# Kernel optimization log

Measured on AMD Instinct MI355X. Metric: run time of the kernel, lower is better.

Reference implementation:

```python
import jax, jax.numpy as jnp
import numpy as np

H = 256
N = 64           # d_state; diagonal SSM uses N//2 conjugate-pair modes
N2 = N // 2
B, L = 16, 4096
EPS = 1e-5


def layernorm(x, g, b):
    m = jnp.mean(x, axis=-1, keepdims=True)
    v = jnp.mean((x - m) ** 2, axis=-1, keepdims=True)
    return (x - m) / jnp.sqrt(v + EPS) * g + b


def s4_layer(u, log_dt, A_re, A_im, C_re, C_im, D, Wout, bout):
    # u: (B, L, H). Bidirectional diagonal S4 (S4D-style ZOH kernel), channels=1.
    Bb, Ll, Hh = u.shape
    dt = jnp.exp(log_dt)                       # (H,)
    A = A_re + 1j * A_im                       # (H, N2), Re(A) < 0
    dtA = dt[:, None] * A                      # (H, N2)
    # ZOH discretization folded into C:  C <- C * (exp(dtA) - 1) / A
    C = (C_re + 1j * C_im) * (jnp.exp(dtA) - 1.0) / A   # (2, H, N2)
    vand = jnp.exp(dtA[:, :, None] * jnp.arange(Ll))    # (H, N2, L)
    k = 2.0 * jnp.einsum('chn,hnl->chl', C, vand).real  # (2, H, L)
    k_fwd, k_bwd = k[0], k[1]
    # bidirectional: causal kernel + anticausal (flipped, shifted by L)
    z = jnp.zeros_like(k_fwd)
    k2 = jnp.concatenate([k_fwd, z], axis=-1) \
       + jnp.concatenate([z, k_bwd[:, ::-1]], axis=-1)  # (H, 2L)
    ut = jnp.transpose(u, (0, 2, 1))                    # (B, H, L)
    n_fft = 2 * Ll
    y = jnp.fft.irfft(jnp.fft.rfft(ut, n=n_fft) * jnp.fft.rfft(k2, n=n_fft), n=n_fft)[..., :Ll]
    y = y + ut * D[:, None]                             # skip connection
    y = jax.nn.gelu(y, approximate=False)
    y = jnp.transpose(y, (0, 2, 1))                     # (B, L, H)
    zz = y @ Wout + bout                                # (B, L, 2H)
    return zz[..., :Hh] * jax.nn.sigmoid(zz[..., Hh:])  # GLU output projection


def setup_inputs() -> dict:
    key = jax.random.key(0)
    ks = jax.random.split(key, 16)
    x = jax.random.normal(ks[0], (B, L, H), dtype=jnp.float32)
    log_dt = jnp.log(0.001) + jax.random.uniform(ks[1], (H,)) * (jnp.log(0.1) - jnp.log(0.001))
    A_re = -0.5 * jnp.ones((H, N2), dtype=jnp.float32)
    A_im = jnp.pi * jnp.broadcast_to(jnp.arange(N2, dtype=jnp.float32), (H, N2))
    C_re = jax.random.normal(ks[2], (2, H, N2), dtype=jnp.float32) * 0.5
    C_im = jax.random.normal(ks[3], (2, H, N2), dtype=jnp.float32) * 0.5
    Dskip = jax.random.normal(ks[4], (H,), dtype=jnp.float32)
    Wout = jax.random.normal(ks[5], (H, 2 * H), dtype=jnp.float32) / np.sqrt(H)
    bout = jnp.zeros((2 * H,), dtype=jnp.float32)
    ln1_g = jnp.ones((H,), jnp.float32); ln1_b = jnp.zeros((H,), jnp.float32)
    ln2_g = jnp.ones((H,), jnp.float32); ln2_b = jnp.zeros((H,), jnp.float32)
    W2 = jax.random.normal(ks[6], (H, 2 * H), dtype=jnp.float32) / np.sqrt(H)
    b2 = jnp.zeros((2 * H,), jnp.float32)
    W3 = jax.random.normal(ks[7], (2 * H, H), dtype=jnp.float32) / np.sqrt(2 * H)
    b3 = jnp.zeros((H,), jnp.float32)
    return dict(x=x, ln1_g=ln1_g, ln1_b=ln1_b, ln2_g=ln2_g, ln2_b=ln2_b,
                log_dt=log_dt, A_re=A_re, A_im=A_im, C_re=C_re, C_im=C_im,
                Dskip=Dskip, Wout=Wout, bout=bout, W2=W2, b2=b2, W3=W3, b3=b3)


def reference(x, ln1_g, ln1_b, ln2_g, ln2_b, log_dt, A_re, A_im, C_re, C_im,
              Dskip, Wout, bout, W2, b2, W3, b3):
    # residual S4 sub-block
    y = x
    h = layernorm(x, ln1_g, ln1_b)
    h = s4_layer(h, log_dt, A_re, A_im, C_re, C_im, Dskip, Wout, bout)
    x = y + h
    # residual MLP sub-block
    y = x
    h = layernorm(x, ln2_g, ln2_b)
    h = jax.nn.gelu(h @ W2 + b2, approximate=False)
    h = h @ W3 + b3
    return y + h
```

## Files before the change

### kernel.cpp

```cpp
#include <hip/hip_runtime.h>
#include <hip/hip_bf16.h>

typedef __attribute__((ext_vector_type(8))) short bf16x8;
typedef __attribute__((ext_vector_type(4))) float f32x4;

#define Hdim 256
#define NM 32
#define NB 16
#define LL 4096
#define PCH 256
#define NCH 16

#define OFF_Q    ((size_t)0)
#define OFF_KC   ((size_t)16777216)
#define OFF_WPM  ((size_t)50331648)
#define OFF_UT   ((size_t)67108864)
#define OFF_ZG   ((size_t)100663296)
#define OFF_M    ((size_t)67108864)
#define OFF_ZP   ((size_t)134217728)
#define OFF_G    ((size_t)150994944)
#define OFF_WTAB ((size_t)185073664)
#define OFF_WPT  ((size_t)185139200)
#define OFF_CE   ((size_t)185204736)
#define OFF_W1T  ((size_t)185335808)
#define OFF_W2T  ((size_t)185597952)
#define OFF_W3T  ((size_t)185860096)

typedef const __attribute__((address_space(1))) void* gas_p;
typedef __attribute__((address_space(3))) void* las_p;

__device__ __forceinline__ float gelu_f(float v) {
    float u = 0.7978845608028654f * fmaf(0.044715f * v * v, v, v);
    float uc = fminf(fmaxf(u, -15.f), 15.f);
    float e = __expf(2.f * uc);
    return 0.5f * v * (1.f + (e - 1.f) * __builtin_amdgcn_rcpf(e + 1.f));
}
__device__ __forceinline__ unsigned short f2bf(float f) {
    unsigned int u = __float_as_uint(f);
    u += 0x7fffu + ((u >> 16) & 1u);
    return (unsigned short)(u >> 16);
}
__device__ __forceinline__ float bf2f(unsigned short u) {
    return __uint_as_float((unsigned int)u << 16);
}

__device__ __forceinline__ bf16x8 fr(const unsigned short* lds, int row, int kcol) {
    return *(const bf16x8*)(lds + row * 64 + ((((kcol >> 3) ^ (row & 7)) << 3)));
}

template<int ROWS, int THREADS>
__device__ __forceinline__ void stage64(const unsigned short* __restrict__ src, int ld, int k0,
                                        unsigned short* lds, int t) {
    constexpr int EPI = THREADS * 8;
#pragma unroll
    for (int i = 0; i < (ROWS * 64) / EPI; i++) {
        int e = i * EPI + t * 8;
        int r = e >> 6;
        int k = (((e >> 3) & 7) ^ (r & 7)) << 3;
        const unsigned short* g = src + (size_t)r * ld + (k0 + k);
        unsigned short* l = lds + i * EPI + (t >> 6) * 512;
        __builtin_amdgcn_global_load_lds((gas_p)g, (las_p)l, 16, 0, 0);
    }
}

template<int ROWS, int THREADS>
__device__ __forceinline__ void stageUT(const unsigned short* __restrict__ UT, int h, int rbase,
                                        int k0, unsigned short* lds, int t) {
    constexpr int EPI = THREADS * 8;
#pragma unroll
    for (int i = 0; i < (ROWS * 64) / EPI; i++) {
        int e = i * EPI + t * 8;
        int r = e >> 6;
        int k = (((e >> 3) & 7) ^ (r & 7)) << 3;
        int row = rbase + r;
        const unsigned short* g = UT + ((size_t)((row >> 4) * Hdim + h)) * LL
                                  + (row & 15) * PCH + (k0 + k);
        unsigned short* l = lds + i * EPI + (t >> 6) * 512;
        __builtin_amdgcn_global_load_lds((gas_p)g, (las_p)l, 16, 0, 0);
    }
}

__global__ void k_tab(const float* __restrict__ logdt, const float* __restrict__ Are,
                      const float* __restrict__ Aim, const float* __restrict__ Cre,
                      const float* __restrict__ Cim, float2* __restrict__ wtab,
                      float2* __restrict__ wptab, float2* __restrict__ ceff) {
    int idx = blockIdx.x * blockDim.x + threadIdx.x;
    if (idx >= Hdim * NM) return;
    int h = idx >> 5;
    float dt = expf(logdt[h]);
    double dar = (double)dt * (double)Are[idx];
    double dai = (double)dt * (double)Aim[idx];
    double wm = exp(dar);
    double wr = wm * cos(dai), wi = wm * sin(dai);
    wtab[idx] = make_float2((float)wr, (float)wi);
    double pm = exp(dar * (double)PCH);
    double pai = dai * (double)PCH;
    wptab[idx] = make_float2((float)(pm * cos(pai)), (float)(pm * sin(pai)));
    double are = (double)Are[idx], aim = (double)Aim[idx];
    double den = are * are + aim * aim;
    double nr = wr - 1.0, ni = wi;
    double qr = (nr * are + ni * aim) / den;
    double qi = (ni * are - nr * aim) / den;
    for (int ch = 0; ch < 2; ch++) {
        double cr = (double)Cre[ch * Hdim * NM + idx];
        double ci = (double)Cim[ch * Hdim * NM + idx];
        ceff[ch * Hdim * NM + idx] = make_float2((float)(cr * qr - ci * qi),
                                                 (float)(cr * qi + ci * qr));
    }
}

__global__ void k_wt(const float* __restrict__ W1, const float* __restrict__ W2,
                     const float* __restrict__ W3, unsigned short* __restrict__ W1T,
                     unsigned short* __restrict__ W2T, unsigned short* __restrict__ W3T) {
    int t = blockIdx.x * 256 + threadIdx.x;
    int k = t >> 9, n = t & 511;
    W1T[n * 256 + k] = f2bf(W1[t]);
    W2T[n * 256 + k] = f2bf(W2[t]);
    int k3 = t >> 8, n3 = t & 255;
    W3T[n3 * 512 + k3] = f2bf(W3[t]);
}

__global__ __launch_bounds__(256) void k_abw(const float* __restrict__ logdt,
                                             const float* __restrict__ Are,
                                             const float* __restrict__ Aim,
                                             const float2* __restrict__ CE,
                                             unsigned short* __restrict__ Q,
                                             unsigned short* __restrict__ Wp,
                                             float* __restrict__ Kcat) {
    __shared__ float2 wpow[32][258];
    __shared__ float2 ce_s[64];
    int h = blockIdx.x;
    int part = blockIdx.y;
    int t = threadIdx.x;
    if (t < 64) ce_s[t] = CE[(t >> 5) * (Hdim * NM) + h * NM + (t & 31)];
    {
        int n = t >> 3, seg = t & 7;
        float dt = expf(logdt[h]);
        float dar = dt * Are[h * NM + n], dai = dt * Aim[h * NM + n];
        float em = expf(dar);
        float wr = em * cosf(dai), wi = em * sinf(dai);
        float ar = wr, ai = wi;
#pragma unroll
        for (int s = 0; s < 3; s++) { float nr = ar * ar - ai * ai, ni = 2.f * ar * ai; ar = nr; ai = ni; }
        float m = expf((float)seg * dar), ang = (float)seg * dai;
        float vr = m * cosf(ang), vi = m * sinf(ang);
        for (int q = 0; q < 32; q++) {
            wpow[n][seg + 8 * q] = make_float2(vr, vi);
            float nr2 = vr * ar - vi * ai;
            float ni2 = vr * ai + vi * ar;
            vr = nr2; vi = ni2;
        }
        if (seg == 0) wpow[n][256] = make_float2(vr, vi);
    }
    __syncthreads();
    if (part == 4) {
        float kfv = 0.f, kbv = 0.f;
#pragma unroll
        for (int n = 0; n < NM; n++) {
            float2 wv = wpow[n][t];
            float2 cf = ce_s[n], cb = ce_s[32 + n];
            kfv = fmaf(cf.x, wv.x, fmaf(-cf.y, wv.y, kfv));
            kbv = fmaf(cb.x, wv.x, fmaf(-cb.y, wv.y, kbv));
        }
        Kcat[(size_t)h * 512 + 255 + t] = 2.f * kfv;
        if (t < 255) Kcat[(size_t)h * 512 + 254 - t] = 2.f * kbv;
        if (t == 255) Kcat[(size_t)h * 512 + 511] = 0.f;
        return;
    }
    for (int jj = 0; jj < 32; jj++) {
        int j = part * 64 + jj * 2 + (t >> 7);
        int tq = t & 127;
        int n = (tq & 63) >> 1, reim = tq & 1;
        float2 c = (tq < 64) ? ce_s[n] : ce_s[32 + n];
        float2 wv = (tq < 64) ? wpow[n][j + 1] : wpow[n][255 - j];
        float re = c.x * wv.x - c.y * wv.y;
        float im = c.x * wv.y + c.y * wv.x;
        Q[((size_t)h * 256 + j) * 128 + tq] = f2bf(reim ? -2.f * im : 2.f * re);
    }
    for (int rr = 0; rr < 32; rr++) {
        int r = part * 32 + rr;
        int n = (r & 63) >> 1, reim = r & 1, dir = r >> 6;
        float2 wv = wpow[n][dir ? t : 255 - t];
        Wp[((size_t)h * 128 + r) * 256 + t] = f2bf(reim ? wv.y : wv.x);
    }
}

__global__ __launch_bounds__(256) void k_lntr(const float* __restrict__ x,
                                              const float* __restrict__ g,
                                              const float* __restrict__ bt,
                                              unsigned short* __restrict__ UT) {
    __shared__ unsigned short lds[256][65];
    int lt = blockIdx.x, b = blockIdx.y;
    int t = threadIdx.x;
    int lane = t & 63, w = t >> 6;
    float4 gg = ((const float4*)g)[lane];
    float4 bb = ((const float4*)bt)[lane];
#pragma unroll
    for (int q = 0; q < 16; q++) {
        int l = q * 4 + w;
        float4 v = ((const float4*)(x + ((size_t)(b * LL + lt * 64 + l)) * Hdim))[lane];
        float s = v.x + v.y + v.z + v.w;
        float ss = v.x * v.x + v.y * v.y + v.z * v.z + v.w * v.w;
#pragma unroll
        for (int o = 1; o < 64; o <<= 1) { s += __shfl_xor(s, o, 64); ss += __shfl_xor(ss, o, 64); }
        float mean = s * (1.0f / Hdim);
        float var = ss * (1.0f / Hdim) - mean * mean;
        float rstd = rsqrtf(var + 1e-5f);
        lds[lane * 4 + 0][l] = f2bf((v.x - mean) * rstd * gg.x + bb.x);
        lds[lane * 4 + 1][l] = f2bf((v.y - mean) * rstd * gg.y + bb.y);
        lds[lane * 4 + 2][l] = f2bf((v.z - mean) * rstd * gg.z + bb.z);
        lds[lane * 4 + 3][l] = f2bf((v.w - mean) * rstd * gg.w + bb.w);
    }
    __syncthreads();
    for (int q = 0; q < 64; q++) {
        int idx = q * 256 + t;
        int hh = idx >> 6, ll = idx & 63;
        UT[((size_t)(b * Hdim + hh)) * LL + lt * 64 + ll] = lds[hh][ll];
    }
}

__global__ void k_ln_bf(const unsigned short* __restrict__ x, const float* __restrict__ g,
                        const float* __restrict__ bt, unsigned short* __restrict__ out) {
    int row = blockIdx.x * 4 + (threadIdx.x >> 6);
    int lane = threadIdx.x & 63;
    ushort4 u4 = ((const ushort4*)(x + (size_t)row * Hdim))[lane];
    float vx = bf2f(u4.x), vy = bf2f(u4.y), vz = bf2f(u4.z), vw = bf2f(u4.w);
    float s = vx + vy + vz + vw;
    float ss = vx * vx + vy * vy + vz * vz + vw * vw;
#pragma unroll
    for (int o = 1; o < 64; o <<= 1) { s += __shfl_xor(s, o, 64); ss += __shfl_xor(ss, o, 64); }
    float mean = s * (1.0f / Hdim);
    float var = ss * (1.0f / Hdim) - mean * mean;
    float rstd = rsqrtf(var + 1e-5f);
    float4 gg = ((const float4*)g)[lane];
    float4 bb = ((const float4*)bt)[lane];
    ushort4 o;
    o.x = f2bf((vx - mean) * rstd * gg.x + bb.x);
    o.y = f2bf((vy - mean) * rstd * gg.y + bb.y);
    o.z = f2bf((vz - mean) * rstd * gg.z + bb.z);
    o.w = f2bf((vw - mean) * rstd * gg.w + bb.w);
    ((ushort4*)(out + (size_t)row * Hdim))[lane] = o;
}

__global__ __launch_bounds__(512) void k_zgemm(const unsigned short* __restrict__ UT,
                                               const unsigned short* __restrict__ Wp,
                                               float* __restrict__ Zg) {
    __shared__ unsigned short As[256 * 64];
    __shared__ unsigned short Bs[128 * 64];
    int h = blockIdx.x;
    int t = threadIdx.x;
    int w = t >> 6, lane = t & 63;
    int m0 = (w & 3) * 64;
    int nb = (w >> 2) * 64;
    int lr = lane & 15, lk = (lane >> 4) * 8;
    f32x4 acc[4][4];
#pragma unroll
    for (int i = 0; i < 4; i++)
#pragma unroll
        for (int jx = 0; jx < 4; jx++) acc[i][jx] = (f32x4){0.f, 0.f, 0.f, 0.f};
    for (int k0 = 0; k0 < 256; k0 += 64) {
        stageUT<256, 512>(UT, h, 0, k0, As, t);
        stage64<128, 512>(Wp + (size_t)h * 128 * 256, 256, k0, Bs, t);
        __syncthreads();
#pragma unroll
        for (int kk = 0; kk < 64; kk += 32) {
            bf16x8 a[4], b[4];
#pragma unroll
            for (int mi = 0; mi < 4; mi++) a[mi] = fr(As, m0 + mi * 16 + lr, kk + lk);
#pragma unroll
            for (int nf = 0; nf < 4; nf++) b[nf] = fr(Bs, nb + nf * 16 + lr, kk + lk);
#pragma unroll
            for (int mi = 0; mi < 4; mi++)
#pragma unroll
                for (int nf = 0; nf < 4; nf++)
                    acc[mi][nf] = __builtin_amdgcn_mfma_f32_16x16x32_bf16(a[mi], b[nf], acc[mi][nf], 0, 0, 0);
        }
        __syncthreads();
    }
#pragma unroll
    for (int mi = 0; mi < 4; mi++)
#pragma unroll
        for (int nf = 0; nf < 4; nf++) {
            int col = nb + nf * 16 + lr;
#pragma unroll
            for (int r = 0; r < 4; r++) {
                int row = m0 + mi * 16 + (lane >> 4) * 4 + r;
                Zg[((size_t)h * 256 + row) * 128 + col] = acc[mi][nf][r];
            }
        }
}

__global__ void k_prefix2(const float* __restrict__ Zg, const float2* __restrict__ wptab,
                          unsigned short* __restrict__ ZP) {
    int t = blockIdx.x * 256 + threadIdx.x;
    int n = t & 31;
    int h = (t >> 5) & 255;
    int b = (t >> 13) & 15;
    int dir = (t >> 17) & 1;
    float2 wp = wptab[h * NM + n];
    float sr = 0.f, si = 0.f;
    int ro = dir ? 64 + 2 * n : 2 * n;
    if (dir == 0) {
        for (int c = 0; c < NCH; c++) {
            size_t base = ((size_t)h * 256 + b * NCH + c) * 128;
            ZP[base + ro] = f2bf(sr);
            ZP[base + ro + 1] = f2bf(si);
            float zr = Zg[base + ro], zi = Zg[base + ro + 1];
            float nr = fmaf(wp.x, sr, fmaf(-wp.y, si, zr));
            float ni = fmaf(wp.y, sr, fmaf(wp.x, si, zi));
            sr = nr; si = ni;
        }
    } else {
        for (int c = NCH - 1; c >= 0; c--) {
            size_t base = ((size_t)h * 256 + b * NCH + c) * 128;
            ZP[base + ro] = f2bf(sr);
            ZP[base + ro + 1] = f2bf(si);
            float zr = Zg[base + ro], zi = Zg[base + ro + 1];
            float nr = fmaf(wp.x, sr, fmaf(-wp.y, si, zr));
            float ni = fmaf(wp.y, sr, fmaf(wp.x, si, zi));
            sr = nr; si = ni;
        }
    }
}

__global__ __launch_bounds__(512) void k_conv(const unsigned short* __restrict__ UT,
                                              const unsigned short* __restrict__ ZP,
                                              const unsigned short* __restrict__ Q,
                                              const float* __restrict__ Kcat,
                                              const float* __restrict__ Dsk,
                                              unsigned short* __restrict__ Yt) {
    __shared__ unsigned short As[128 * 64];
    __shared__ unsigned short Bs[256 * 64];
    __shared__ float kcs[512];
    int wgid = ((int)blockIdx.x % 8) * 64 + (int)blockIdx.x / 8;
    int h = wgid >> 1;
    int mbase = (wgid & 1) * 128;
    int t = threadIdx.x;
    int w = t >> 6, lane = t & 63;
    int m0 = (w & 1) * 64;
    int nb = (w >> 1) * 64;
    int lr = lane & 15, lk = (lane >> 4) * 8;
    float dsk = Dsk[h];
    kcs[t] = Kcat[(size_t)h * 512 + t];
    __syncthreads();
    f32x4 acc[4][4];
#pragma unroll
    for (int i = 0; i < 4; i++)
#pragma unroll
        for (int jx = 0; jx < 4; jx++) acc[i][jx] = (f32x4){0.f, 0.f, 0.f, 0.f};
    for (int k0 = 0; k0 < 256; k0 += 64) {
        stageUT<128, 512>(UT, h, mbase, k0, As, t);
#pragma unroll
        for (int gq = 0; gq < 4; gq++) {
            int e = gq * 4096 + t * 8;
            int j = e >> 6;
            int i0 = k0 + (e & 63);
            union { bf16x8 v; unsigned short u[8]; } pk;
#pragma unroll
            for (int q = 0; q < 8; q++) {
                int i = i0 + q;
                float f = kcs[255 + j - i];
                if (i == j) f += dsk;
                pk.u[q] = f2bf(f);
            }
            *(bf16x8*)(Bs + j * 64 + (((((e & 63) >> 3)) ^ (j & 7)) << 3)) = pk.v;
        }
        __syncthreads();
#pragma unroll
        for (int kk = 0; kk < 64; kk += 32) {
            bf16x8 a[4], b[4];
#pragma unroll
            for (int mi = 0; mi < 4; mi++) a[mi] = fr(As, m0 + mi * 16 + lr, kk + lk);
#pragma unroll
            for (int nf = 0; nf < 4; nf++) b[nf] = fr(Bs, nb + nf * 16 + lr, kk + lk);
#pragma unroll
            for (int mi = 0; mi < 4; mi++)
#pragma unroll
                for (int nf = 0; nf < 4; nf++)
                    acc[mi][nf] = __builtin_amdgcn_mfma_f32_16x16x32_bf16(a[mi], b[nf], acc[mi][nf], 0, 0, 0);
        }
        __syncthreads();
    }
    for (int k0 = 0; k0 < 128; k0 += 64) {
        stage64<128, 512>(ZP + ((size_t)h * 256 + mbase) * 128, 128, k0, As, t);
        stage64<256, 512>(Q + (size_t)h * 256 * 128, 128, k0, Bs, t);
        __syncthreads();
#pragma unroll
        for (int kk = 0; kk < 64; kk += 32) {
            bf16x8 a[4], b[4];
#pragma unroll
            for (int mi = 0; mi < 4; mi++) a[mi] = fr(As, m0 + mi * 16 + lr, kk + lk);
#pragma unroll
            for (int nf = 0; nf < 4; nf++) b[nf] = fr(Bs, nb + nf * 16 + lr, kk + lk);
#pragma unroll
            for (int mi = 0; mi < 4; mi++)
#pragma unroll
                for (int nf = 0; nf < 4; nf++)
                    acc[mi][nf] = __builtin_amdgcn_mfma_f32_16x16x32_bf16(a[mi], b[nf], acc[mi][nf], 0, 0, 0);
        }
        __syncthreads();
    }
#pragma unroll
    for (int mi = 0; mi < 4; mi++)
#pragma unroll
        for (int nf = 0; nf < 4; nf++) {
            int col = nb + nf * 16 + lr;
#pragma unroll
            for (int r = 0; r < 4; r++) {
                int row = mbase + m0 + mi * 16 + (lane >> 4) * 4 + r;
                Yt[(size_t)h * 65536 + row * 256 + col] = f2bf(gelu_f(acc[mi][nf][r]));
            }
        }
}

__global__ void k_trg(const unsigned short* __restrict__ Yt, unsigned short* __restrict__ G) {
    __shared__ unsigned short lds[64][65];
    int bc = blockIdx.x;
    int h0 = blockIdx.y * 64, j0 = blockIdx.z * 64;
    int t = threadIdx.x;
#pragma unroll
    for (int q = 0; q < 16; q++) {
        int idx = q * 256 + t;
        int hh = idx >> 6, jj = idx & 63;
        lds[hh][jj] = Yt[(size_t)(h0 + hh) * 65536 + bc * 256 + j0 + jj];
    }
    __syncthreads();
    int b = bc >> 4, c = bc & 15;
#pragma unroll
    for (int q = 0; q < 16; q++) {
        int idx = q * 256 + t;
        int jj = idx >> 6, hh = idx & 63;
        G[((size_t)(b * LL + c * PCH + j0 + jj)) * Hdim + h0 + hh] = lds[hh][jj];
    }
}

__global__ __launch_bounds__(512) void k_gemm1(const unsigned short* __restrict__ Gm,
                                               const unsigned short* __restrict__ W1T,
                                               const float* __restrict__ bo,
                                               const float* __restrict__ xin,
                                               unsigned short* __restrict__ X2) {
    __shared__ unsigned short As[128 * 64];
    __shared__ unsigned short BsA[128 * 64];
    __shared__ unsigned short BsB[128 * 64];
    int t = threadIdx.x;
    int w = t >> 6, lane = t & 63;
    int m0w = (w & 1) * 64;
    int n0w = (w >> 1) * 32;
    int lr = lane & 15, lk = (lane >> 4) * 8;
    int mblk = blockIdx.x * 128, nblk = blockIdx.y * 128;
    const unsigned short* Ab  = Gm + (size_t)mblk * 256;
    const unsigned short* BbA = W1T + (size_t)nblk * 256;
    const unsigned short* BbB = W1T + (size_t)(nblk + 256) * 256;
    f32x4 acc[4][4];
#pragma unroll
    for (int i = 0; i < 4; i++)
#pragma unroll
        for (int j = 0; j < 4; j++) acc[i][j] = (f32x4){0.f, 0.f, 0.f, 0.f};
    for (int k0 = 0; k0 < 256; k0 += 64) {
        stage64<128, 512>(Ab, 256, k0, As, t);
        stage64<128, 512>(BbA, 256, k0, BsA, t);
        stage64<128, 512>(BbB, 256, k0, BsB, t);
        __syncthreads();
#pragma unroll
        for (int kk = 0; kk < 64; kk += 32) {
            bf16x8 a[4], bA[2], bB[2];
#pragma unroll
            for (int mi = 0; mi < 4; mi++)
                a[mi] = fr(As, m0w + mi * 16 + lr, kk + lk);
#pragma unroll
            for (int nf = 0; nf < 2; nf++) {
                bA[nf] = fr(BsA, n0w + nf * 16 + lr, kk + lk);
                bB[nf] = fr(BsB, n0w + nf * 16 + lr, kk + lk);
            }
#pragma unroll
            for (int mi = 0; mi < 4; mi++)
#pragma unroll
                for (int nf = 0; nf < 2; nf++) {
                    acc[mi][nf] = __builtin_amdgcn_mfma_f32_16x16x32_bf16(a[mi], bA[nf], acc[mi][nf], 0, 0, 0);
                    acc[mi][nf + 2] = __builtin_amdgcn_mfma_f32_16x16x32_bf16(a[mi], bB[nf], acc[mi][nf + 2], 0, 0, 0);
                }
        }
        __syncthreads();
    }
#pragma unroll
    for (int mi = 0; mi < 4; mi++)
#pragma unroll
        for (int nf = 0; nf < 2; nf++) {
            int col = nblk + n0w + nf * 16 + lr;
            float biasA = bo[col], biasB = bo[col + 256];
#pragma unroll
            for (int r = 0; r < 4; r++) {
                int row = mblk + m0w + mi * 16 + (lane >> 4) * 4 + r;
                float zzA = acc[mi][nf][r] + biasA;
                float zzB = acc[mi][nf + 2][r] + biasB;
                float v = zzA * __builtin_amdgcn_rcpf(1.0f + __expf(-zzB));
                size_t idx = (size_t)row * 256 + col;
                X2[idx] = f2bf(xin[idx] + v);
            }
        }
}

__global__ __launch_bounds__(512) void k_gemm2(const unsigned short* __restrict__ T2,
                                               const unsigned short* __restrict__ W2T,
                                               const float* __restrict__ b2,
                                               unsigned short* __restrict__ Mo) {
    __shared__ unsigned short As[128 * 64];
    __shared__ unsigned short Bs[256 * 64];
    int t = threadIdx.x;
    int w = t >> 6, lane = t & 63;
    int m0w = (w & 1) * 64;
    int n0w = (w >> 1) * 64;
    int lr = lane & 15, lk = (lane >> 4) * 8;
    int mblk = blockIdx.x * 128, nblk = blockIdx.y * 256;
    const unsigned short* Ab = T2 + (size_t)mblk * 256;
    const unsigned short* Bb = W2T + (size_t)nblk * 256;
    f32x4 acc[4][4];
#pragma unroll
    for (int i = 0; i < 4; i++)
#pragma unroll
        for (int j = 0; j < 4; j++) acc[i][j] = (f32x4){0.f, 0.f, 0.f, 0.f};
    for (int k0 = 0; k0 < 256; k0 += 64) {
        stage64<128, 512>(Ab, 256, k0, As, t);
        stage64<256, 512>(Bb, 256, k0, Bs, t);
        __syncthreads();
#pragma unroll
        for (int kk = 0; kk < 64; kk += 32) {
            bf16x8 a[4], b[4];
#pragma unroll
            for (int mi = 0; mi < 4; mi++)
                a[mi] = fr(As, m0w + mi * 16 + lr, kk + lk);
#pragma unroll
            for (int nf = 0; nf < 4; nf++)
                b[nf] = fr(Bs, n0w + nf * 16 + lr, kk + lk);
#pragma unroll
            for (int mi = 0; mi < 4; mi++)
#pragma unroll
                for (int nf = 0; nf < 4; nf++)
                    acc[mi][nf] = __builtin_amdgcn_mfma_f32_16x16x32_bf16(a[mi], b[nf], acc[mi][nf], 0, 0, 0);
        }
        __syncthreads();
    }
#pragma unroll
    for (int mi = 0; mi < 4; mi++)
#pragma unroll
        for (int nf = 0; nf < 4; nf++) {
            int col = nblk + n0w + nf * 16 + lr;
            float bias = b2[col];
#pragma unroll
            for (int r = 0; r < 4; r++) {
                int row = mblk + m0w + mi * 16 + (lane >> 4) * 4 + r;
                Mo[(size_t)row * 512 + col] = f2bf(gelu_f(acc[mi][nf][r] + bias));
            }
        }
}

__global__ __launch_bounds__(512) void k_gemm3(const unsigned short* __restrict__ Mb,
                                               const unsigned short* __restrict__ W3T,
                                               const float* __restrict__ b3,
                                               const unsigned short* __restrict__ X2,
                                               float* __restrict__ out) {
    __shared__ unsigned short As[128 * 64];
    __shared__ unsigned short Bs[256 * 64];
    int t = threadIdx.x;
    int w = t >> 6, lane = t & 63;
    int m0w = (w & 1) * 64;
    int n0w = (w >> 1) * 64;
    int lr = lane & 15, lk = (lane >> 4) * 8;
    int mblk = blockIdx.x * 128;
    const unsigned short* Ab = Mb + (size_t)mblk * 512;
    f32x4 acc[4][4];
#pragma unroll
    for (int i = 0; i < 4; i++)
#pragma unroll
        for (int j = 0; j < 4; j++) acc[i][j] = (f32x4){0.f, 0.f, 0.f, 0.f};
    for (int k0 = 0; k0 < 512; k0 += 64) {
        stage64<128, 512>(Ab, 512, k0, As, t);
        stage64<256, 512>(W3T, 512, k0, Bs, t);
        __syncthreads();
#pragma unroll
        for (int kk = 0; kk < 64; kk += 32) {
            bf16x8 a[4], b[4];
#pragma unroll
            for (int mi = 0; mi < 4; mi++)
                a[mi] = fr(As, m0w + mi * 16 + lr, kk + lk);
#pragma unroll
            for (int nf = 0; nf < 4; nf++)
                b[nf] = fr(Bs, n0w + nf * 16 + lr, kk + lk);
#pragma unroll
            for (int mi = 0; mi < 4; mi++)
#pragma unroll
                for (int nf = 0; nf < 4; nf++)
                    acc[mi][nf] = __builtin_amdgcn_mfma_f32_16x16x32_bf16(a[mi], b[nf], acc[mi][nf], 0, 0, 0);
        }
        __syncthreads();
    }
#pragma unroll
    for (int mi = 0; mi < 4; mi++)
#pragma unroll
        for (int nf = 0; nf < 4; nf++) {
            int col = n0w + nf * 16 + lr;
            float bias = b3[col];
#pragma unroll
            for (int r = 0; r < 4; r++) {
                int row = mblk + m0w + mi * 16 + (lane >> 4) * 4 + r;
                size_t idx = (size_t)row * 256 + col;
                out[idx] = bf2f(X2[idx]) + acc[mi][nf][r] + bias;
            }
        }
}

extern "C" void kernel_launch(void* const* d_in, const int* in_sizes, int n_in,
                              void* d_out, int out_size, void* d_ws, size_t ws_size,
                              hipStream_t stream) {
    const float* x     = (const float*)d_in[0];
    const float* ln1g  = (const float*)d_in[1];
    const float* ln1b  = (const float*)d_in[2];
    const float* ln2g  = (const float*)d_in[3];
    const float* ln2b  = (const float*)d_in[4];
    const float* logdt = (const float*)d_in[5];
    const float* Are   = (const float*)d_in[6];
    const float* Aim   = (const float*)d_in[7];
    const float* Cre   = (const float*)d_in[8];
    const float* Cim   = (const float*)d_in[9];
    const float* Dsk   = (const float*)d_in[10];
    const float* Wout  = (const float*)d_in[11];
    const float* bo    = (const float*)d_in[12];
    const float* W2    = (const float*)d_in[13];
    const float* b2    = (const float*)d_in[14];
    const float* W3    = (const float*)d_in[15];
    const float* b3    = (const float*)d_in[16];

    char* ws = (char*)d_ws;
    unsigned short* Q    = (unsigned short*)(ws + OFF_Q);
    float*          Kc   = (float*)(ws + OFF_KC);
    unsigned short* Wp   = (unsigned short*)(ws + OFF_WPM);
    unsigned short* X2   = (unsigned short*)(ws + OFF_Q);
    unsigned short* UT   = (unsigned short*)(ws + OFF_UT);
    float*          Zg   = (float*)(ws + OFF_ZG);
    unsigned short* Yt   = (unsigned short*)(ws + OFF_ZG);
    unsigned short* Mb   = (unsigned short*)(ws + OFF_M);
    unsigned short* ZP   = (unsigned short*)(ws + OFF_ZP);
    unsigned short* G    = (unsigned short*)(ws + OFF_G);
    float2*         WT   = (float2*)(ws + OFF_WTAB);
    float2*         WPT  = (float2*)(ws + OFF_WPT);
    float2*         CE   = (float2*)(ws + OFF_CE);
    unsigned short* W1T  = (unsigned short*)(ws + OFF_W1T);
    unsigned short* W2T  = (unsigned short*)(ws + OFF_W2T);
    unsigned short* W3T  = (unsigned short*)(ws + OFF_W3T);

    k_tab<<<32, 256, 0, stream>>>(logdt, Are, Aim, Cre, Cim, WT, WPT, CE);
    k_wt<<<512, 256, 0, stream>>>(Wout, W2, W3, W1T, W2T, W3T);
    k_lntr<<<dim3(64, 16), 256, 0, stream>>>(x, ln1g, ln1b, UT);
    k_abw<<<dim3(256, 5), 256, 0, stream>>>(logdt, Are, Aim, CE, Q, Wp, Kc);
    k_zgemm<<<256, 512, 0, stream>>>(UT, Wp, Zg);
    k_prefix2<<<1024, 256, 0, stream>>>(Zg, WPT, ZP);
    k_conv<<<512, 512, 0, stream>>>(UT, ZP, Q, Kc, Dsk, Yt);
    k_trg<<<dim3(256, 4, 4), 256, 0, stream>>>(Yt, G);
    k_gemm1<<<dim3(512, 2), 512, 0, stream>>>(G, W1T, bo, x, X2);
    k_ln_bf<<<NB * LL / 4, 256, 0, stream>>>(X2, ln2g, ln2b, G);
    k_gemm2<<<dim3(512, 2), 512, 0, stream>>>(G, W2T, b2, Mb);
    k_gemm3<<<512, 512, 0, stream>>>(Mb, W3T, b3, X2, (float*)d_out);
}
```

Before: 238.9 us.

## Widen dense GEMM blocks to full N with 1024 threads; store Zg as bf16

The three MLP/GLU GEMMs now each launch 1024-thread blocks that cover the full output width. This replaces the earlier 2D grids, so the A tile is loaded once per row block instead of once per column block, at the cost of larger LDS tiles and lower occupancy. k_gemm3 uses 16 waves with a smaller per-wave N tile. The chunk-state intermediate Zg is also written as bf16 instead of fp32, which halves traffic between k_zgemm and k_prefix2 but loses precision in the scan inputs.

```diff
diff --git a/kernel.cpp b/kernel.cpp
--- a/kernel.cpp
+++ b/kernel.cpp
@@ -244,7 +244,7 @@
 
 __global__ __launch_bounds__(512) void k_zgemm(const unsigned short* __restrict__ UT,
                                                const unsigned short* __restrict__ Wp,
-                                               float* __restrict__ Zg) {
+                                               unsigned short* __restrict__ Zg) {
     __shared__ unsigned short As[256 * 64];
     __shared__ unsigned short Bs[128 * 64];
     int h = blockIdx.x;
@@ -285,12 +285,12 @@
 #pragma unroll
             for (int r = 0; r < 4; r++) {
                 int row = m0 + mi * 16 + (lane >> 4) * 4 + r;
-                Zg[((size_t)h * 256 + row) * 128 + col] = acc[mi][nf][r];
+                Zg[((size_t)h * 256 + row) * 128 + col] = f2bf(acc[mi][nf][r]);
             }
         }
 }
 
-__global__ void k_prefix2(const float* __restrict__ Zg, const float2* __restrict__ wptab,
+__global__ void k_prefix2(const unsigned short* __restrict__ Zg, const float2* __restrict__ wptab,
                           unsigned short* __restrict__ ZP) {
     int t = blockIdx.x * 256 + threadIdx.x;
     int n = t & 31;
@@ -305,7 +305,7 @@
             size_t base = ((size_t)h * 256 + b * NCH + c) * 128;
             ZP[base + ro] = f2bf(sr);
             ZP[base + ro + 1] = f2bf(si);
-            float zr = Zg[base + ro], zi = Zg[base + ro + 1];
+            float zr = bf2f(Zg[base + ro]), zi = bf2f(Zg[base + ro + 1]);
             float nr = fmaf(wp.x, sr, fmaf(-wp.y, si, zr));
             float ni = fmaf(wp.y, sr, fmaf(wp.x, si, zi));
             sr = nr; si = ni;
@@ -315,7 +315,7 @@
             size_t base = ((size_t)h * 256 + b * NCH + c) * 128;
             ZP[base + ro] = f2bf(sr);
             ZP[base + ro + 1] = f2bf(si);
-            float zr = Zg[base + ro], zi = Zg[base + ro + 1];
+            float zr = bf2f(Zg[base + ro]), zi = bf2f(Zg[base + ro + 1]);
             float nr = fmaf(wp.x, sr, fmaf(-wp.y, si, zr));
             float ni = fmaf(wp.y, sr, fmaf(wp.x, si, zi));
             sr = nr; si = ni;
@@ -434,32 +434,30 @@
     }
 }
 
-__global__ __launch_bounds__(512) void k_gemm1(const unsigned short* __restrict__ Gm,
-                                               const unsigned short* __restrict__ W1T,
-                                               const float* __restrict__ bo,
-                                               const float* __restrict__ xin,
-                                               unsigned short* __restrict__ X2) {
+__global__ __launch_bounds__(1024) void k_gemm1(const unsigned short* __restrict__ Gm,
+                                                const unsigned short* __restrict__ W1T,
+                                                const float* __restrict__ bo,
+                                                const float* __restrict__ xin,
+                                                unsigned short* __restrict__ X2) {
     __shared__ unsigned short As[128 * 64];
-    __shared__ unsigned short BsA[128 * 64];
-    __shared__ unsigned short BsB[128 * 64];
+    __shared__ unsigned short BsA[256 * 64];
+    __shared__ unsigned short BsB[256 * 64];
     int t = threadIdx.x;
     int w = t >> 6, lane = t & 63;
     int m0w = (w & 1) * 64;
     int n0w = (w >> 1) * 32;
     int lr = lane & 15, lk = (lane >> 4) * 8;
-    int mblk = blockIdx.x * 128, nblk = blockIdx.y * 128;
+    int mblk = blockIdx.x * 128;
     const unsigned short* Ab  = Gm + (size_t)mblk * 256;
-    const unsigned short* BbA = W1T + (size_t)nblk * 256;
-    const unsigned short* BbB = W1T + (size_t)(nblk + 256) * 256;
     f32x4 acc[4][4];
 #pragma unroll
     for (int i = 0; i < 4; i++)
 #pragma unroll
         for (int j = 0; j < 4; j++) acc[i][j] = (f32x4){0.f, 0.f, 0.f, 0.f};
     for (int k0 = 0; k0 < 256; k0 += 64) {
-        stage64<128, 512>(Ab, 256, k0, As, t);
-        stage64<128, 512>(BbA, 256, k0, BsA, t);
-        stage64<128, 512>(BbB, 256, k0, BsB, t);
+        stage64<128, 1024>(Ab, 256, k0, As, t);
+        stage64<256, 1024>(W1T, 256, k0, BsA, t);
+        stage64<256, 1024>(W1T + (size_t)256 * 256, 256, k0, BsB, t);
         __syncthreads();
 #pragma unroll
         for (int kk = 0; kk < 64; kk += 32) {
@@ -486,7 +484,7 @@
     for (int mi = 0; mi < 4; mi++)
 #pragma unroll
         for (int nf = 0; nf < 2; nf++) {
-            int col = nblk + n0w + nf * 16 + lr;
+            int col = n0w + nf * 16 + lr;
             float biasA = bo[col], biasB = bo[col + 256];
 #pragma unroll
             for (int r = 0; r < 4; r++) {
@@ -500,82 +498,27 @@
         }
 }
 
-__global__ __launch_bounds__(512) void k_gemm2(const unsigned short* __restrict__ T2,
-                                               const unsigned short* __restrict__ W2T,
-                                               const float* __restrict__ b2,
-                                               unsigned short* __restrict__ Mo) {
+__global__ __launch_bounds__(1024) void k_gemm2(const unsigned short* __restrict__ T2,
+                                                const unsigned short* __restrict__ W2T,
+                                                const float* __restrict__ b2,
+                                                unsigned short* __restrict__ Mo) {
     __shared__ unsigned short As[128 * 64];
-    __shared__ unsigned short Bs[256 * 64];
-    int t = threadIdx.x;
-    int w = t >> 6, lane = t & 63;
-    int m0w = (w & 1) * 64;
-    int n0w = (w >> 1) * 64;
-    int lr = lane & 15, lk = (lane >> 4) * 8;
-    int mblk = blockIdx.x * 128, nblk = blockIdx.y * 256;
-    const unsigned short* Ab = T2 + (size_t)mblk * 256;
-    const unsigned short* Bb = W2T + (size_t)nblk * 256;
-    f32x4 acc[4][4];
-#pragma unroll
-    for (int i = 0; i < 4; i++)
-#pragma unroll
-        for (int j = 0; j < 4; j++) acc[i][j] = (f32x4){0.f, 0.f, 0.f, 0.f};
-    for (int k0 = 0; k0 < 256; k0 += 64) {
-        stage64<128, 512>(Ab, 256, k0, As, t);
-        stage64<256, 512>(Bb, 256, k0, Bs, t);
-        __syncthreads();
-#pragma unroll
-        for (int kk = 0; kk < 64; kk += 32) {
-            bf16x8 a[4], b[4];
-#pragma unroll
-            for (int mi = 0; mi < 4; mi++)
-                a[mi] = fr(As, m0w + mi * 16 + lr, kk + lk);
-#pragma unroll
-            for (int nf = 0; nf < 4; nf++)
-                b[nf] = fr(Bs, n0w + nf * 16 + lr, kk + lk);
-#pragma unroll
-            for (int mi = 0; mi < 4; mi++)
-#pragma unroll
-                for (int nf = 0; nf < 4; nf++)
-                    acc[mi][nf] = __builtin_amdgcn_mfma_f32_16x16x32_bf16(a[mi], b[nf], acc[mi][nf], 0, 0, 0);
-        }
-        __syncthreads();
-    }
-#pragma unroll
-    for (int mi = 0; mi < 4; mi++)
-#pragma unroll
-        for (int nf = 0; nf < 4; nf++) {
-            int col = nblk + n0w + nf * 16 + lr;
-            float bias = b2[col];
-#pragma unroll
-            for (int r = 0; r < 4; r++) {
-                int row = mblk + m0w + mi * 16 + (lane >> 4) * 4 + r;
-                Mo[(size_t)row * 512 + col] = f2bf(gelu_f(acc[mi][nf][r] + bias));
-            }
-        }
-}
-
-__global__ __launch_bounds__(512) void k_gemm3(const unsigned short* __restrict__ Mb,
-                                               const unsigned short* __restrict__ W3T,
-                                               const float* __restrict__ b3,
-                                               const unsigned short* __restrict__ X2,
-                                               float* __restrict__ out) {
-    __shared__ unsigned short As[128 * 64];
-    __shared__ unsigned short Bs[256 * 64];
+    __shared__ unsigned short Bs[512 * 64];
     int t = threadIdx.x;
     int w = t >> 6, lane = t & 63;
     int m0w = (w & 1) * 64;
     int n0w = (w >> 1) * 64;
     int lr = lane & 15, lk = (lane >> 4) * 8;
     int mblk = blockIdx.x * 128;
-    const unsigned short* Ab = Mb + (size_t)mblk * 512;
+    const unsigned short* Ab = T2 + (size_t)mblk * 256;
     f32x4 acc[4][4];
 #pragma unroll
     for (int i = 0; i < 4; i++)
 #pragma unroll
         for (int j = 0; j < 4; j++) acc[i][j] = (f32x4){0.f, 0.f, 0.f, 0.f};
-    for (int k0 = 0; k0 < 512; k0 += 64) {
-        stage64<128, 512>(Ab, 512, k0, As, t);
-        stage64<256, 512>(W3T, 512, k0, Bs, t);
+    for (int k0 = 0; k0 < 256; k0 += 64) {
+        stage64<128, 1024>(Ab, 256, k0, As, t);
+        stage64<512, 1024>(W2T, 256, k0, Bs, t);
         __syncthreads();
 #pragma unroll
         for (int kk = 0; kk < 64; kk += 32) {
@@ -598,6 +541,58 @@
     for (int mi = 0; mi < 4; mi++)
 #pragma unroll
         for (int nf = 0; nf < 4; nf++) {
+            int col = n0w + nf * 16 + lr;
+            float bias = b2[col];
+#pragma unroll
+            for (int r = 0; r < 4; r++) {
+                int row = mblk + m0w + mi * 16 + (lane >> 4) * 4 + r;
+                Mo[(size_t)row * 512 + col] = f2bf(gelu_f(acc[mi][nf][r] + bias));
+            }
+        }
+}
+
+__global__ __launch_bounds__(1024) void k_gemm3(const unsigned short* __restrict__ Mb,
+                                                const unsigned short* __restrict__ W3T,
+                                                const float* __restrict__ b3,
+                                                const unsigned short* __restrict__ X2,
+                                                float* __restrict__ out) {
+    __shared__ unsigned short As[128 * 64];
+    __shared__ unsigned short Bs[256 * 64];
+    int t = threadIdx.x;
+    int w = t >> 6, lane = t & 63;
+    int m0w = (w & 1) * 64;
+    int n0w = (w >> 1) * 32;
+    int lr = lane & 15, lk = (lane >> 4) * 8;
+    int mblk = blockIdx.x * 128;
+    const unsigned short* Ab = Mb + (size_t)mblk * 512;
+    f32x4 acc[4][2];
+#pragma unroll
+    for (int i = 0; i < 4; i++) { acc[i][0] = (f32x4){0.f,0.f,0.f,0.f}; acc[i][1] = (f32x4){0.f,0.f,0.f,0.f}; }
+    for (int k0 = 0; k0 < 512; k0 += 64) {
+        stage64<128, 1024>(Ab, 512, k0, As, t);
+        stage64<256, 1024>(W3T, 512, k0, Bs, t);
+        __syncthreads();
+#pragma unroll
+        for (int kk = 0; kk < 64; kk += 32) {
+            bf16x8 a[4], b[2];
+#pragma unroll
+            for (int mi = 0; mi < 4; mi++)
+                a[mi] = fr(As, m0w + mi * 16 + lr, kk + lk);
+#pragma unroll
+            for (int nf = 0; nf < 2; nf++)
+                b[nf] = fr(Bs, n0w + nf * 16 + lr, kk + lk);
+#pragma unroll
+            for (int mi = 0; mi < 4; mi++)
+#pragma unroll
+                for (int nf = 0; nf < 2; nf++)
+                    acc[mi][nf] = __builtin_amdgcn_mfma_f32_16x16x32_bf16(a[mi], b[nf], acc[mi][nf], 0, 0, 0);
+        }
+        __syncthreads();
+    }
+#pragma unroll
+    for (int mi = 0; mi < 4; mi++)
+#pragma unroll
+        for (int nf = 0; nf < 2; nf++) {
             int col = n0w + nf * 16 + lr;
             float bias = b3[col];
 #pragma unroll
@@ -636,7 +631,7 @@
     unsigned short* Wp   = (unsigned short*)(ws + OFF_WPM);
     unsigned short* X2   = (unsigned short*)(ws + OFF_Q);
     unsigned short* UT   = (unsigned short*)(ws + OFF_UT);
-    float*          Zg   = (float*)(ws + OFF_ZG);
+    unsigned short* Zg   = (unsigned short*)(ws + OFF_ZG);
     unsigned short* Yt   = (unsigned short*)(ws + OFF_ZG);
     unsigned short* Mb   = (unsigned short*)(ws + OFF_M);
     unsigned short* ZP   = (unsigned short*)(ws + OFF_ZP);
@@ -656,8 +651,8 @@
     k_prefix2<<<1024, 256, 0, stream>>>(Zg, WPT, ZP);
     k_conv<<<512, 512, 0, stream>>>(UT, ZP, Q, Kc, Dsk, Yt);
     k_trg<<<dim3(256, 4, 4), 256, 0, stream>>>(Yt, G);
-    k_gemm1<<<dim3(512, 2), 512, 0, stream>>>(G, W1T, bo, x, X2);
+    k_gemm1<<<512, 1024, 0, stream>>>(G, W1T, bo, x, X2);
     k_ln_bf<<<NB * LL / 4, 256, 0, stream>>>(X2, ln2g, ln2b, G);
-    k_gemm2<<<dim3(512, 2), 512, 0, stream>>>(G, W2T, b2, Mb);
-    k_gemm3<<<512, 512, 0, stream>>>(Mb, W3T, b3, X2, (float*)d_out);
-}
+    k_gemm2<<<512, 1024, 0, stream>>>(G, W2T, b2, Mb);
+    k_gemm3<<<512, 1024, 0, stream>>>(Mb, W3T, b3, X2, (float*)d_out);
+}
```

Measured after the change: 234.7 us (median of 3 runs). No clear change (-1.8%).
